# Performance work log

Hardware: AMD Instinct MI355X
Metric: run time of the kernel (lower is better)

Reference implementation:

```python
import jax, jax.numpy as jnp
import numpy as np

QUERY_SIZE = 128


def setup_inputs() -> dict:
    key = jax.random.key(0)
    ks = jax.random.split(key, 4)
    S, B, T, E, Q = 512, 32, 1024, 512, QUERY_SIZE
    query = jax.random.normal(ks[0], (S, B, Q), dtype=jnp.float32)
    embedded_text = jax.random.normal(ks[1], (T, B, E), dtype=jnp.float32)
    text_mask = jnp.ones((T, B), dtype=jnp.float32)
    position = jnp.zeros((S, B), dtype=jnp.float32)
    # nn.Linear(query_size, 2): W [2, Q], b [2]; kaiming-uniform-ish init scale
    lim = 1.0 / np.sqrt(Q)
    W = jax.random.uniform(ks[2], (2, Q), dtype=jnp.float32, minval=-lim, maxval=lim)
    b = jax.random.uniform(ks[3], (2,), dtype=jnp.float32, minval=-lim, maxval=lim)
    return {"query": query, "embedded_text": embedded_text, "text_mask": text_mask,
            "position": position, "W": W, "b": b}


def reference(query, embedded_text, text_mask, position, W, b):
    # query: [S,B,Q], embedded_text: [T,B,E], text_mask: [T,B], position: [S,B]
    masked_embedding = embedded_text * text_mask[:, :, None]          # [T,B,E]
    query_result = jnp.exp(query @ W.T + b)                           # [S,B,2]
    mean_raw = query_result[..., 0]                                   # [S,B]
    std = query_result[..., 1]                                        # [S,B]
    mean = position + jnp.cumsum(mean_raw, axis=0) / 20.0             # [S,B]
    T = embedded_text.shape[0]
    indices = jnp.arange(T, dtype=query.dtype)                        # [T]
    # Gaussian window weights over text positions: [S,T,B]
    weights = jnp.exp(-std[:, None, :] * (mean[:, None, :] - indices[None, :, None]) ** 2)
    # Reduce over text_len without materializing [S,T,B,E]
    new_context = jnp.einsum('stb,tbe->sbe', weights, masked_embedding)  # [S,B,E]
    return new_context, mean
```

## Files before the change

### kernel.cpp

```cpp
#include <hip/hip_runtime.h>
#include <hip/hip_bf16.h>


#define S_DIM 512
#define B_DIM 32
#define T_DIM 1024
#define E_DIM 512
#define Q_DIM 128
#define WIN_CUT 20.0f
#define CH 16
#define TSEG 64

typedef float v4f __attribute__((ext_vector_type(4)));

__global__ __launch_bounds__(256) void dot_kernel(
    const float* __restrict__ query,
    const float* __restrict__ W,
    const float* __restrict__ bias,
    float* __restrict__ ws_mraw,
    float* __restrict__ ws_std)
{
    const int wave = threadIdx.x >> 6;
    const int lane = threadIdx.x & 63;
    const int pair = blockIdx.x * 4 + wave;
    const float2* qp = (const float2*)(query + (size_t)pair * Q_DIM);
    float2 v = qp[lane];
    float d0 = v.x * W[2 * lane]         + v.y * W[2 * lane + 1];
    float d1 = v.x * W[Q_DIM + 2 * lane] + v.y * W[Q_DIM + 2 * lane + 1];
    #pragma unroll
    for (int off = 32; off; off >>= 1) {
        d0 += __shfl_down(d0, off);
        d1 += __shfl_down(d1, off);
    }
    if (lane == 0) {
        int s = pair / B_DIM, b = pair % B_DIM;
        ws_mraw[(size_t)b * S_DIM + s] = expf(d0 + bias[0]);
        ws_std[(size_t)b * S_DIM + s]  = expf(d1 + bias[1]);
    }
}

__global__ __launch_bounds__(256) void ctx_kernel(
    const float* __restrict__ emb,
    const float* __restrict__ mask,
    const float* __restrict__ ws_mraw,
    const float* __restrict__ ws_std,
    const float* __restrict__ position,
    float* __restrict__ out,
    float* __restrict__ out_mean)
{
    __shared__ float lds_w[TSEG * CH];
    __shared__ float lds_mean[CH], lds_std[CH];
    __shared__ float lds_lo[CH], lds_hi[CH];
    __shared__ float lds_wt[4];
    __shared__ int s_tlo, s_thi;
    const int c = blockIdx.x, b = blockIdx.y;
    const int s0 = c * CH;
    const int tid = threadIdx.x;
    const int wv = tid >> 6, lane = tid & 63;
    const int half = tid >> 7;
    const int htid = tid & 127;

    float2 f2 = ((const float2*)(ws_mraw + (size_t)b * S_DIM))[tid];
    float sc = f2.x + f2.y;
    #pragma unroll
    for (int off = 1; off < 64; off <<= 1) {
        float u = __shfl_up(sc, off);
        if (lane >= off) sc += u;
    }
    if (lane == 63) lds_wt[wv] = sc;
    __syncthreads();
    float woff = 0.f;
    #pragma unroll
    for (int w = 0; w < 4; ++w) woff += (w < wv) ? lds_wt[w] : 0.f;
    if (tid >= (s0 >> 1) && tid < ((s0 + CH) >> 1)) {
        const int i0 = tid * 2 - s0;
        const int sa = s0 + i0, sb = sa + 1;
        float m0 = position[(size_t)sa * B_DIM + b] + (woff + sc - f2.y) * 0.05f;
        float m1 = position[(size_t)sb * B_DIM + b] + (woff + sc) * 0.05f;
        float sd0 = ws_std[(size_t)b * S_DIM + sa];
        float sd1 = ws_std[(size_t)b * S_DIM + sb];
        lds_mean[i0] = m0;  lds_mean[i0 + 1] = m1;
        lds_std[i0]  = sd0; lds_std[i0 + 1]  = sd1;
        float r0 = __fsqrt_rn(WIN_CUT / sd0);
        float r1 = __fsqrt_rn(WIN_CUT / sd1);
        lds_lo[i0] = m0 - r0; lds_hi[i0] = m0 + r0;
        lds_lo[i0 + 1] = m1 - r1; lds_hi[i0 + 1] = m1 + r1;
        out_mean[(size_t)sa * B_DIM + b] = m0;
        out_mean[(size_t)sb * B_DIM + b] = m1;
    }
    __syncthreads();
    if (tid == 0) {
        float lo = 1e30f, hi = -1e30f;
        #pragma unroll
        for (int i = 0; i < CH; ++i) {
            lo = fminf(lo, lds_lo[i]);
            hi = fmaxf(hi, lds_hi[i]);
        }
        int tlo = (int)floorf(lo);
        if (tlo < 0) tlo = 0; if (tlo > T_DIM - 1) tlo = T_DIM - 1;
        int thi = (int)ceilf(hi);
        if (thi > T_DIM - 1) thi = T_DIM - 1; if (thi < tlo) thi = tlo;
        s_tlo = tlo; s_thi = thi;
    }
    __syncthreads();
    const int tlo = s_tlo, thi = s_thi;

    v4f acc[8];
    #pragma unroll
    for (int i = 0; i < 8; ++i) acc[i] = (v4f)0.f;

    for (int tseg = tlo; tseg <= thi; tseg += TSEG) {
        {
            const int toff = tid >> 2;
            const int ibase = (tid & 3) * 4;
            const int t = tseg + toff;
            float mv = 0.f;
            if (t <= thi) mv = mask[(size_t)t * B_DIM + b];
            v4f w;
            #pragma unroll
            for (int j = 0; j < 4; ++j) {
                int i = ibase + j;
                float d = lds_mean[i] - (float)t;
                w[j] = (t <= thi) ? __expf(-lds_std[i] * d * d) * mv : 0.f;
            }
            *(v4f*)(lds_w + toff * CH + ibase) = w;
        }
        __syncthreads();
        const int tend = (thi < tseg + TSEG - 1) ? thi : (tseg + TSEG - 1);
        const float* wbase = lds_w + half * 8;
        v4f v = ((const v4f*)(emb + ((size_t)tseg * B_DIM + b) * E_DIM))[htid];
        for (int t = tseg; t <= tend; ++t) {
            const int tn = (t < tend) ? t + 1 : t;
            v4f vn = ((const v4f*)(emb + ((size_t)tn * B_DIM + b) * E_DIM))[htid];
            const float* wrow = wbase + (t - tseg) * CH;
            #pragma unroll
            for (int i = 0; i < 8; ++i) {
                float w = wrow[i];
                acc[i] += w * v;
            }
            v = vn;
        }
        __syncthreads();
    }
    #pragma unroll
    for (int i = 0; i < 8; ++i) {
        v4f* dst = (v4f*)(out + ((size_t)(s0 + half * 8 + i) * B_DIM + b) * E_DIM);
        __builtin_nontemporal_store(acc[i], dst + htid);
    }
}

extern "C" void kernel_launch(void* const* d_in, const int* in_sizes, int n_in,
                              void* d_out, int out_size, void* d_ws, size_t ws_size,
                              hipStream_t stream) {
    const float* query = (const float*)d_in[0];
    const float* emb   = (const float*)d_in[1];
    const float* mask  = (const float*)d_in[2];
    const float* pos   = (const float*)d_in[3];
    const float* W     = (const float*)d_in[4];
    const float* bias  = (const float*)d_in[5];

    float* out_ctx  = (float*)d_out;
    float* out_mean = out_ctx + (size_t)S_DIM * B_DIM * E_DIM;

    float* ws_mraw = (float*)d_ws;
    float* ws_std  = ws_mraw + (size_t)S_DIM * B_DIM;

    dot_kernel<<<(S_DIM * B_DIM) / 4, 256, 0, stream>>>(query, W, bias, ws_mraw, ws_std);
    ctx_kernel<<<dim3(S_DIM / CH, B_DIM), 256, 0, stream>>>(
        emb, mask, ws_mraw, ws_std, pos, out_ctx, out_mean);
}
```

Baseline: 125.6 us.

## Fuse query projection into context kernel with cooperative grid sync

```diff
diff --git a/kernel.cpp b/kernel.cpp
--- a/kernel.cpp
+++ b/kernel.cpp
@@ -1,5 +1,7 @@
 #include <hip/hip_runtime.h>
-#include <hip/hip_bf16.h>
+#include <hip/hip_cooperative_groups.h>
+
+namespace cg = cooperative_groups;
 
 
 #define S_DIM 512
@@ -13,38 +15,15 @@
 
 typedef float v4f __attribute__((ext_vector_type(4)));
 
-__global__ __launch_bounds__(256) void dot_kernel(
+__global__ __launch_bounds__(256, 4) void fused_kernel(
     const float* __restrict__ query,
     const float* __restrict__ W,
     const float* __restrict__ bias,
-    float* __restrict__ ws_mraw,
-    float* __restrict__ ws_std)
-{
-    const int wave = threadIdx.x >> 6;
-    const int lane = threadIdx.x & 63;
-    const int pair = blockIdx.x * 4 + wave;
-    const float2* qp = (const float2*)(query + (size_t)pair * Q_DIM);
-    float2 v = qp[lane];
-    float d0 = v.x * W[2 * lane]         + v.y * W[2 * lane + 1];
-    float d1 = v.x * W[Q_DIM + 2 * lane] + v.y * W[Q_DIM + 2 * lane + 1];
-    #pragma unroll
-    for (int off = 32; off; off >>= 1) {
-        d0 += __shfl_down(d0, off);
-        d1 += __shfl_down(d1, off);
-    }
-    if (lane == 0) {
-        int s = pair / B_DIM, b = pair % B_DIM;
-        ws_mraw[(size_t)b * S_DIM + s] = expf(d0 + bias[0]);
-        ws_std[(size_t)b * S_DIM + s]  = expf(d1 + bias[1]);
-    }
-}
-
-__global__ __launch_bounds__(256) void ctx_kernel(
     const float* __restrict__ emb,
     const float* __restrict__ mask,
-    const float* __restrict__ ws_mraw,
-    const float* __restrict__ ws_std,
     const float* __restrict__ position,
+    float* __restrict__ ws_mraw,
+    float* __restrict__ ws_std,
     float* __restrict__ out,
     float* __restrict__ out_mean)
 {
@@ -59,6 +38,34 @@
     const int wv = tid >> 6, lane = tid & 63;
     const int half = tid >> 7;
     const int htid = tid & 127;
+
+    {
+        float2 qv[4];
+        #pragma unroll
+        for (int k = 0; k < 4; ++k) {
+            const int s = s0 + wv * 4 + k;
+            qv[k] = ((const float2*)(query + ((size_t)s * B_DIM + b) * Q_DIM))[lane];
+        }
+        const float w0a = W[2 * lane],         w0b = W[2 * lane + 1];
+        const float w1a = W[Q_DIM + 2 * lane], w1b = W[Q_DIM + 2 * lane + 1];
+        const float b0 = bias[0], b1 = bias[1];
+        #pragma unroll
+        for (int k = 0; k < 4; ++k) {
+            float d0 = qv[k].x * w0a + qv[k].y * w0b;
+            float d1 = qv[k].x * w1a + qv[k].y * w1b;
+            #pragma unroll
+            for (int off = 32; off; off >>= 1) {
+                d0 += __shfl_down(d0, off);
+                d1 += __shfl_down(d1, off);
+            }
+            if (lane == 0) {
+                const int s = s0 + wv * 4 + k;
+                ws_mraw[(size_t)b * S_DIM + s] = expf(d0 + b0);
+                ws_std[(size_t)b * S_DIM + s]  = expf(d1 + b1);
+            }
+        }
+    }
+    cg::this_grid().sync();
 
     float2 f2 = ((const float2*)(ws_mraw + (size_t)b * S_DIM))[tid];
     float sc = f2.x + f2.y;
@@ -165,7 +172,12 @@
     float* ws_mraw = (float*)d_ws;
     float* ws_std  = ws_mraw + (size_t)S_DIM * B_DIM;
 
-    dot_kernel<<<(S_DIM * B_DIM) / 4, 256, 0, stream>>>(query, W, bias, ws_mraw, ws_std);
-    ctx_kernel<<<dim3(S_DIM / CH, B_DIM), 256, 0, stream>>>(
-        emb, mask, ws_mraw, ws_std, pos, out_ctx, out_mean);
+    void* args[] = {
+        (void*)&query, (void*)&W, (void*)&bias, (void*)&emb, (void*)&mask,
+        (void*)&pos, (void*)&ws_mraw, (void*)&ws_std, (void*)&out_ctx,
+        (void*)&out_mean
+    };
+    hipLaunchCooperativeKernel((const void*)fused_kernel,
+                               dim3(S_DIM / CH, B_DIM), dim3(256, 1, 1),
+                               args, 0, stream);
 }
```

New measurement: 212.3 us. +69.1%, slower.
